# Kernel tuning notes

Hardware: AMD Instinct MI355X
Metric: run time of the kernel (lower is better)

## Reference

```python
import jax, jax.numpy as jnp
import numpy as np

DIM = 1024
HEADS = 16
HEAD_DIM = DIM // HEADS
SCALE = HEAD_DIM ** -0.5


def setup_inputs() -> dict:
    key = jax.random.key(0)
    ks = jax.random.split(key, 7)
    B, N, M = 2, 2048, 2048
    x = jax.random.normal(ks[0], (B, N, DIM), dtype=jnp.float32)
    y = jax.random.normal(ks[1], (B, M, DIM), dtype=jnp.float32)
    s = DIM ** -0.5
    Wq = jax.random.normal(ks[2], (DIM, DIM), dtype=jnp.float32) * s
    Wk = jax.random.normal(ks[3], (DIM, DIM), dtype=jnp.float32) * s
    Wv = jax.random.normal(ks[4], (DIM, DIM), dtype=jnp.float32) * s
    Wp = jax.random.normal(ks[5], (DIM, DIM), dtype=jnp.float32) * s
    bp = jax.random.normal(ks[6], (DIM,), dtype=jnp.float32) * 0.01
    return {"x": x, "y": y, "Wq": Wq, "Wk": Wk, "Wv": Wv, "Wp": Wp, "bp": bp}


def _split_heads(t):
    b, n, _ = t.shape
    return t.reshape(b, n, HEADS, HEAD_DIM).transpose(0, 2, 1, 3)  # b h n d


def reference(x, y, Wq, Wk, Wv, Wp, bp):
    q = _split_heads(x @ Wq)  # [b,h,n,d]
    k = _split_heads(y @ Wk)  # [b,h,m,d]
    v = _split_heads(y @ Wv)  # [b,h,m,d]
    attn = jnp.einsum('bhid,bhjd->bhij', q, k) * SCALE  # [b,h,n,m]
    attn = jax.nn.softmax(attn, axis=-1)
    out = jnp.einsum('bhij,bhjd->bhid', attn, v)  # [b,h,n,d]
    b, h, n, d = out.shape
    out = out.transpose(0, 2, 1, 3).reshape(b, n, h * d)  # [b,n,dim]
    return out @ Wp + bp
```

## Files before the change

kernel.cpp:

```cpp
#include <hip/hip_runtime.h>
#include <hip/hip_bf16.h>
#include <cstdint>

#define DIM   1024
#define HEADS 16
#define HDIM  64
#define BATCH 2
#define SEQ   2048
#define ROWS  (BATCH*SEQ)
static constexpr float QSCALE = 0.18033688f;

typedef float  f32x4  __attribute__((ext_vector_type(4)));
typedef float  float4v __attribute__((ext_vector_type(4)));
typedef __bf16 bf16x8 __attribute__((ext_vector_type(8)));
typedef __bf16 bf16x4 __attribute__((ext_vector_type(4)));
typedef short  short4v __attribute__((ext_vector_type(4)));

#if __has_builtin(__builtin_amdgcn_mfma_f32_16x16x16_bf16)
__device__ __forceinline__ f32x4 mfma16(bf16x4 a, bf16x4 b, f32x4 c) {
  return __builtin_amdgcn_mfma_f32_16x16x16_bf16(a, b, c, 0, 0, 0);
}
#else
__device__ __forceinline__ f32x4 mfma16(bf16x4 a, bf16x4 b, f32x4 c) {
  return __builtin_amdgcn_mfma_f32_16x16x16bf16_1k(
      __builtin_bit_cast(short4v, a), __builtin_bit_cast(short4v, b), c, 0, 0, 0);
}
#endif

__device__ __forceinline__ void glds16(const __bf16* g, __bf16* l) {
  __builtin_amdgcn_global_load_lds(
      (const __attribute__((address_space(1))) void*)g,
      (__attribute__((address_space(3))) void*)l, 16, 0, 0);
}

__global__ __launch_bounds__(256) void prep_kernel(
    const float* __restrict__ x, const float* __restrict__ y,
    const float* __restrict__ Wq, const float* __restrict__ Wk,
    const float* __restrict__ Wv, const float* __restrict__ Wp,
    __bf16* __restrict__ xb, __bf16* __restrict__ yb, __bf16* __restrict__ Wt) {
  const int z = blockIdx.z, t = threadIdx.x;
  const size_t NEL = (size_t)ROWS * DIM;
  if (z < 8) {
    size_t idx = (((size_t)z * 1024 + blockIdx.x) * 256 + t) * 4;
    const float* s; __bf16* d;
    if (idx < NEL) { s = x + idx; d = xb + idx; }
    else           { s = y + (idx - NEL); d = yb + (idx - NEL); }
    const float4v v = *(const float4v*)s;
    bf16x4 o;
    o[0] = (__bf16)v[0]; o[1] = (__bf16)v[1]; o[2] = (__bf16)v[2]; o[3] = (__bf16)v[3];
    *(bf16x4*)d = o;
    return;
  }
  const int w = blockIdx.x >> 8, rem = blockIdx.x & 255;
  const float* W = (w == 0) ? Wq : (w == 1) ? Wk : (w == 2) ? Wv : Wp;
  __bf16* dst = Wt + (size_t)w * DIM * DIM;
  const int n0 = (rem & 15) * 64, k0 = (rem >> 4) * 64;
  __shared__ float T[64][65];
  const int col = t & 63, rw = t >> 6;
  #pragma unroll
  for (int p = 0; p < 16; ++p) {
    const int row = p * 4 + rw;
    T[row][col] = W[(size_t)(k0 + row) * DIM + n0 + col];
  }
  __syncthreads();
  #pragma unroll
  for (int p = 0; p < 16; ++p) {
    const int row = p * 4 + rw;
    dst[(size_t)(n0 + row) * DIM + k0 + col] = (__bf16)T[col][row];
  }
}

__global__ __launch_bounds__(256) void proj_kernel(
    const __bf16* __restrict__ xb, const __bf16* __restrict__ yb,
    const __bf16* __restrict__ Wt,
    __bf16* __restrict__ Qb, __bf16* __restrict__ Kb, __bf16* __restrict__ VT) {
  const int z = blockIdx.z;
  const __bf16* A = (z == 0) ? xb : yb;
  const __bf16* Bt = Wt + (size_t)z * DIM * DIM;

  __shared__ __bf16 S[2][128 * 64];
  __bf16* As = S[0];
  __bf16* Bs = S[1];

  const int t = threadIdx.x, lane = t & 63, wave = t >> 6;
  const int l15 = lane & 15, quad = lane >> 4;
  const int wm = wave & 1, wn = wave >> 1;
  const int rowBase = blockIdx.y * 128, colBase = blockIdx.x * 128;
  const int srow = lane >> 3;
  const int scol = ((lane & 7) ^ srow) * 8;

  f32x4 acc[4][4] = {};

  for (int kb = 0; kb < DIM; kb += 64) {
    __syncthreads();
    #pragma unroll
    for (int i = 0; i < 4; ++i) {
      const int c = wave * 4 + i;
      const int row = c * 8 + srow;
      glds16(&A[(size_t)(rowBase + row) * DIM + kb + scol], &As[c * 512]);
      glds16(&Bt[(size_t)(colBase + row) * DIM + kb + scol], &Bs[c * 512]);
    }
    __syncthreads();
    #pragma unroll
    for (int ks = 0; ks < 2; ++ks) {
      bf16x8 a[4], b[4];
      #pragma unroll
      for (int mi = 0; mi < 4; ++mi) {
        const int row = wm * 64 + mi * 16 + l15;
        a[mi] = *(const bf16x8*)&As[row * 64 + (((ks << 2) | quad) ^ (row & 7)) * 8];
      }
      #pragma unroll
      for (int ni = 0; ni < 4; ++ni) {
        const int row = wn * 64 + ni * 16 + l15;
        b[ni] = *(const bf16x8*)&Bs[row * 64 + (((ks << 2) | quad) ^ (row & 7)) * 8];
      }
      #pragma unroll
      for (int mi = 0; mi < 4; ++mi)
        #pragma unroll
        for (int ni = 0; ni < 4; ++ni)
          acc[mi][ni] = __builtin_amdgcn_mfma_f32_16x16x32_bf16(a[mi], b[ni], acc[mi][ni], 0, 0, 0);
    }
  }

  if (z < 2) {
    __bf16* out = (z == 0) ? Qb : Kb;
    const float sc = (z == 0) ? QSCALE : 1.0f;
    #pragma unroll
    for (int mi = 0; mi < 4; ++mi) {
      const int row0 = rowBase + wm * 64 + mi * 16 + quad * 4;
      #pragma unroll
      for (int ni = 0; ni < 4; ++ni) {
        const int col = colBase + wn * 64 + ni * 16 + l15;
        #pragma unroll
        for (int r = 0; r < 4; ++r)
          out[(size_t)(row0 + r) * DIM + col] = (__bf16)(acc[mi][ni][r] * sc);
      }
    }
    return;
  }

  __syncthreads();
  __bf16* Ts = &S[0][0];
  #pragma unroll
  for (int mi = 0; mi < 4; ++mi) {
    const int bk3 = wm * 8 + mi * 2 + (quad >> 1);
    #pragma unroll
    for (int ni = 0; ni < 4; ++ni) {
      const int dl = wn * 64 + ni * 16 + l15;
      bf16x4 pk;
      #pragma unroll
      for (int r = 0; r < 4; ++r) pk[r] = (__bf16)acc[mi][ni][r];
      *(bf16x4*)&Ts[dl * 128 + (bk3 ^ (dl & 7)) * 8 + (quad & 1) * 4] = pk;
    }
  }
  __syncthreads();
  const int d = t >> 1, khh = t & 1;
  const size_t vrow = (size_t)((rowBase >> 11) * HEADS * HDIM) + colBase + d;
  const int key0g = rowBase & (SEQ - 1);
  #pragma unroll
  for (int j = 0; j < 8; ++j) {
    const int kc = khh * 8 + j;
    const int lc = (kc & 8) | ((kc ^ d) & 7);
    const bf16x8 v = *(const bf16x8*)&Ts[d * 128 + lc * 8];
    *(bf16x8*)&VT[vrow * SEQ + key0g + kc * 8] = v;
  }
}

__global__ __launch_bounds__(256, 2) void attn_kernel(
    const __bf16* __restrict__ Qb, const __bf16* __restrict__ Kb,
    const __bf16* __restrict__ VT, __bf16* __restrict__ Ob) {
  __shared__ __bf16 KV[2][2][64 * 64];
  __shared__ float lb[2][128];

  const int t = threadIdx.x, lane = t & 63, wave = t >> 6;
  const int l15 = lane & 15, quad = lane >> 4;
  const int bh = blockIdx.y, b = bh >> 4, h = bh & 15;
  const int qseg = wave & 1, kh = wave >> 1;
  const int qrow0 = blockIdx.x * 128 + qseg * 64;
  const int srow = lane >> 3;
  const int scol = ((lane & 7) ^ srow) * 8;

  const __bf16* Kbh = Kb + (size_t)b * SEQ * DIM + h * HDIM;
  const __bf16* Vbh = VT + (size_t)bh * HDIM * SEQ;

  bf16x8 qf[4][2];
  #pragma unroll
  for (int mi = 0; mi < 4; ++mi)
    #pragma unroll
    for (int ks = 0; ks < 2; ++ks)
      qf[mi][ks] = *(const bf16x8*)&Qb[(size_t)(b * SEQ + qrow0 + mi * 16 + l15) * DIM
                                       + h * HDIM + ks * 32 + quad * 8];

  bf16x4 ones4;
  #pragma unroll
  for (int i = 0; i < 4; ++i) ones4[i] = (__bf16)1.0f;

  f32x4 o[4][4] = {};
  f32x4 lacc[4] = {};

  auto stage = [&](int jb, int buf) {
    #pragma unroll
    for (int i = 0; i < 2; ++i) {
      const int c = wave * 2 + i;
      const int row = c * 8 + srow;
      glds16(&Kbh[(size_t)(jb + row) * DIM + scol], &KV[buf][0][c * 512]);
      glds16(&Vbh[(size_t)row * SEQ + jb + scol], &KV[buf][1][c * 512]);
    }
  };

  stage(0, 0);
  for (int j = 0; j < SEQ / 64; ++j) {
    const int buf = j & 1;
    __syncthreads();
    if (j + 1 < SEQ / 64) stage((j + 1) * 64, buf ^ 1);
    const __bf16* Ks = KV[buf][0];
    const __bf16* Vs = KV[buf][1];

    f32x4 sT[2][4] = {};
    #pragma unroll
    for (int ks = 0; ks < 2; ++ks)
      #pragma unroll
      for (int ni = 0; ni < 2; ++ni) {
        const int key = kh * 32 + ni * 16 + l15;
        const bf16x8 kf = *(const bf16x8*)&Ks[key * 64 + (((ks << 2) | quad) ^ (key & 7)) * 8];
        #pragma unroll
        for (int mi = 0; mi < 4; ++mi)
          sT[ni][mi] = __builtin_amdgcn_mfma_f32_16x16x32_bf16(kf, qf[mi][ks], sT[ni][mi], 0, 0, 0);
      }

    bf16x4 pa[2][4];
    #pragma unroll
    for (int ni = 0; ni < 2; ++ni)
      #pragma unroll
      for (int mi = 0; mi < 4; ++mi)
        #pragma unroll
        for (int r = 0; r < 4; ++r)
          pa[ni][mi][r] = (__bf16)__builtin_amdgcn_exp2f(sT[ni][mi][r]);

    #pragma unroll
    for (int ni = 0; ni < 2; ++ni) {
      const int key0 = kh * 32 + ni * 16;
      #pragma unroll
      for (int mi = 0; mi < 4; ++mi)
        lacc[mi] = mfma16(pa[ni][mi], ones4, lacc[mi]);
      #pragma unroll
      for (int dt = 0; dt < 4; ++dt) {
        const int d = dt * 16 + l15;
        const bf16x4 vf = *(const bf16x4*)&Vs[d * 64
            + (((key0 >> 3) + (quad >> 1)) ^ (d & 7)) * 8 + (quad & 1) * 4];
        #pragma unroll
        for (int mi = 0; mi < 4; ++mi)
          o[mi][dt] = mfma16(pa[ni][mi], vf, o[mi][dt]);
      }
    }
  }

  __syncthreads();
  float* mb = (float*)&KV[0][0][0];
  if (l15 == 0) {
    #pragma unroll
    for (int mi = 0; mi < 4; ++mi)
      #pragma unroll
      for (int r = 0; r < 4; ++r)
        lb[kh][qseg * 64 + mi * 16 + quad * 4 + r] = lacc[mi][r];
  }
  if (kh == 1) {
    #pragma unroll
    for (int mi = 0; mi < 4; ++mi)
      #pragma unroll
      for (int r = 0; r < 4; ++r) {
        const int q = mi * 16 + quad * 4 + r;
        #pragma unroll
        for (int dt = 0; dt < 4; ++dt)
          mb[qseg * 4096 + q * 64 + dt * 16 + l15] = o[mi][dt][r];
      }
  }
  __syncthreads();
  if (kh == 0) {
    #pragma unroll
    for (int mi = 0; mi < 4; ++mi)
      #pragma unroll
      for (int r = 0; r < 4; ++r) {
        const int q = mi * 16 + quad * 4 + r;
        const float inv = 1.f / (lb[0][qseg * 64 + q] + lb[1][qseg * 64 + q]);
        const size_t row = (size_t)(b * SEQ + qrow0 + q);
        #pragma unroll
        for (int dt = 0; dt < 4; ++dt) {
          const float ov = o[mi][dt][r] + mb[qseg * 4096 + q * 64 + dt * 16 + l15];
          Ob[row * DIM + h * HDIM + dt * 16 + l15] = (__bf16)(ov * inv);
        }
      }
  }
}

__global__ __launch_bounds__(256) void outproj_kernel(
    const __bf16* __restrict__ A, const __bf16* __restrict__ Bt,
    const float* __restrict__ bias, float* __restrict__ out) {
  __shared__ __bf16 As[64 * 64];
  __shared__ __bf16 Bs[128 * 64];

  const int t = threadIdx.x, lane = t & 63, wave = t >> 6;
  const int l15 = lane & 15, quad = lane >> 4;
  const int wm = wave & 1, wn = wave >> 1;
  const int rowBase = blockIdx.y * 64, colBase = blockIdx.x * 128;
  const int srow = lane >> 3;
  const int scol = ((lane & 7) ^ srow) * 8;

  f32x4 acc[2][4] = {};

  for (int kb = 0; kb < DIM; kb += 64) {
    __syncthreads();
    #pragma unroll
    for (int i = 0; i < 2; ++i) {
      const int c = wave * 2 + i;
      const int row = c * 8 + srow;
      glds16(&A[(size_t)(rowBase + row) * DIM + kb + scol], &As[c * 512]);
    }
    #pragma unroll
    for (int i = 0; i < 4; ++i) {
      const int c = wave * 4 + i;
      const int row = c * 8 + srow;
      glds16(&Bt[(size_t)(colBase + row) * DIM + kb + scol], &Bs[c * 512]);
    }
    __syncthreads();
    #pragma unroll
    for (int ks = 0; ks < 2; ++ks) {
      bf16x8 a[2], b[4];
      #pragma unroll
      for (int mi = 0; mi < 2; ++mi) {
        const int row = wm * 32 + mi * 16 + l15;
        a[mi] = *(const bf16x8*)&As[row * 64 + (((ks << 2) | quad) ^ (row & 7)) * 8];
      }
      #pragma unroll
      for (int ni = 0; ni < 4; ++ni) {
        const int row = wn * 64 + ni * 16 + l15;
        b[ni] = *(const bf16x8*)&Bs[row * 64 + (((ks << 2) | quad) ^ (row & 7)) * 8];
      }
      #pragma unroll
      for (int mi = 0; mi < 2; ++mi)
        #pragma unroll
        for (int ni = 0; ni < 4; ++ni)
          acc[mi][ni] = __builtin_amdgcn_mfma_f32_16x16x32_bf16(a[mi], b[ni], acc[mi][ni], 0, 0, 0);
    }
  }

  #pragma unroll
  for (int mi = 0; mi < 2; ++mi) {
    const int row0 = rowBase + wm * 32 + mi * 16 + quad * 4;
    #pragma unroll
    for (int ni = 0; ni < 4; ++ni) {
      const int col = colBase + wn * 64 + ni * 16 + l15;
      const float bb = bias[col];
      #pragma unroll
      for (int r = 0; r < 4; ++r)
        out[(size_t)(row0 + r) * DIM + col] = acc[mi][ni][r] + bb;
    }
  }
}

extern "C" void kernel_launch(void* const* d_in, const int* in_sizes, int n_in,
                              void* d_out, int out_size, void* d_ws, size_t ws_size,
                              hipStream_t stream) {
  const float* x  = (const float*)d_in[0];
  const float* y  = (const float*)d_in[1];
  const float* Wq = (const float*)d_in[2];
  const float* Wk = (const float*)d_in[3];
  const float* Wv = (const float*)d_in[4];
  const float* Wp = (const float*)d_in[5];
  const float* bp = (const float*)d_in[6];
  float* out = (float*)d_out;

  const size_t NEL = (size_t)ROWS * DIM;
  __bf16* xb = (__bf16*)d_ws;
  __bf16* yb = xb + NEL;
  __bf16* Wt = yb + NEL;
  __bf16* Qb = Wt + NEL;
  __bf16* Kb = Qb + NEL;
  __bf16* VT = Kb + NEL;
  __bf16* Ob = xb;

  prep_kernel<<<dim3(1024, 1, 9), 256, 0, stream>>>(x, y, Wq, Wk, Wv, Wp, xb, yb, Wt);
  proj_kernel<<<dim3(DIM / 128, ROWS / 128, 3), 256, 0, stream>>>(xb, yb, Wt, Qb, Kb, VT);
  attn_kernel<<<dim3(SEQ / 128, BATCH * HEADS), 256, 0, stream>>>(Qb, Kb, VT, Ob);
  outproj_kernel<<<dim3(DIM / 128, ROWS / 64), 256, 0, stream>>>(Ob, Wt + 3 * NEL / 4, bp, out);
}
```

Baseline: 212.4 us.

## Halve attention query tile, raise occupancy, compute row sums via shuffles

Shrinks the per-block query tile in the attention kernel from 128 to 64 rows. This doubles the grid to 1024 blocks, flattened to 1D with heads innermost, and launch bounds ask for 4 blocks per CU. The softmax denominator is now accumulated with scalar adds plus cross-lane shuffles instead of an extra MFMA against a ones vector. The aim is better latency hiding and CU fill, at the cost of each K/V tile being loaded and reused for half as many queries, which doubles K/V traffic.

```diff
diff --git a/kernel.cpp b/kernel.cpp
--- a/kernel.cpp
+++ b/kernel.cpp
@@ -166,37 +166,34 @@
   }
 }
 
-__global__ __launch_bounds__(256, 2) void attn_kernel(
+__global__ __launch_bounds__(256, 4) void attn_kernel(
     const __bf16* __restrict__ Qb, const __bf16* __restrict__ Kb,
     const __bf16* __restrict__ VT, __bf16* __restrict__ Ob) {
   __shared__ __bf16 KV[2][2][64 * 64];
-  __shared__ float lb[2][128];
+  __shared__ float lb[2][64];
 
   const int t = threadIdx.x, lane = t & 63, wave = t >> 6;
   const int l15 = lane & 15, quad = lane >> 4;
-  const int bh = blockIdx.y, b = bh >> 4, h = bh & 15;
+  const int bh = blockIdx.x & 31, qx = blockIdx.x >> 5;
+  const int b = bh >> 4, h = bh & 15;
   const int qseg = wave & 1, kh = wave >> 1;
-  const int qrow0 = blockIdx.x * 128 + qseg * 64;
+  const int qrow0 = qx * 64 + qseg * 32;
   const int srow = lane >> 3;
   const int scol = ((lane & 7) ^ srow) * 8;
 
   const __bf16* Kbh = Kb + (size_t)b * SEQ * DIM + h * HDIM;
   const __bf16* Vbh = VT + (size_t)bh * HDIM * SEQ;
 
-  bf16x8 qf[4][2];
-  #pragma unroll
-  for (int mi = 0; mi < 4; ++mi)
+  bf16x8 qf[2][2];
+  #pragma unroll
+  for (int mi = 0; mi < 2; ++mi)
     #pragma unroll
     for (int ks = 0; ks < 2; ++ks)
       qf[mi][ks] = *(const bf16x8*)&Qb[(size_t)(b * SEQ + qrow0 + mi * 16 + l15) * DIM
                                        + h * HDIM + ks * 32 + quad * 8];
 
-  bf16x4 ones4;
-  #pragma unroll
-  for (int i = 0; i < 4; ++i) ones4[i] = (__bf16)1.0f;
-
-  f32x4 o[4][4] = {};
-  f32x4 lacc[4] = {};
+  f32x4 o[2][4] = {};
+  float lsum[2] = {};
 
   auto stage = [&](int jb, int buf) {
     #pragma unroll
@@ -216,7 +213,7 @@
     const __bf16* Ks = KV[buf][0];
     const __bf16* Vs = KV[buf][1];
 
-    f32x4 sT[2][4] = {};
+    f32x4 sT[2][2] = {};
     #pragma unroll
     for (int ks = 0; ks < 2; ++ks)
       #pragma unroll
@@ -224,69 +221,72 @@
         const int key = kh * 32 + ni * 16 + l15;
         const bf16x8 kf = *(const bf16x8*)&Ks[key * 64 + (((ks << 2) | quad) ^ (key & 7)) * 8];
         #pragma unroll
-        for (int mi = 0; mi < 4; ++mi)
+        for (int mi = 0; mi < 2; ++mi)
           sT[ni][mi] = __builtin_amdgcn_mfma_f32_16x16x32_bf16(kf, qf[mi][ks], sT[ni][mi], 0, 0, 0);
       }
 
-    bf16x4 pa[2][4];
+    bf16x4 pa[2][2];
     #pragma unroll
     for (int ni = 0; ni < 2; ++ni)
       #pragma unroll
-      for (int mi = 0; mi < 4; ++mi)
-        #pragma unroll
-        for (int r = 0; r < 4; ++r)
-          pa[ni][mi][r] = (__bf16)__builtin_amdgcn_exp2f(sT[ni][mi][r]);
+      for (int mi = 0; mi < 2; ++mi)
+        #pragma unroll
+        for (int r = 0; r < 4; ++r) {
+          const float pv = __builtin_amdgcn_exp2f(sT[ni][mi][r]);
+          lsum[mi] += pv;
+          pa[ni][mi][r] = (__bf16)pv;
+        }
 
     #pragma unroll
     for (int ni = 0; ni < 2; ++ni) {
       const int key0 = kh * 32 + ni * 16;
-      #pragma unroll
-      for (int mi = 0; mi < 4; ++mi)
-        lacc[mi] = mfma16(pa[ni][mi], ones4, lacc[mi]);
       #pragma unroll
       for (int dt = 0; dt < 4; ++dt) {
         const int d = dt * 16 + l15;
         const bf16x4 vf = *(const bf16x4*)&Vs[d * 64
             + (((key0 >> 3) + (quad >> 1)) ^ (d & 7)) * 8 + (quad & 1) * 4];
         #pragma unroll
-        for (int mi = 0; mi < 4; ++mi)
+        for (int mi = 0; mi < 2; ++mi)
           o[mi][dt] = mfma16(pa[ni][mi], vf, o[mi][dt]);
       }
     }
   }
 
+  #pragma unroll
+  for (int mi = 0; mi < 2; ++mi) {
+    lsum[mi] += __shfl_xor(lsum[mi], 16, 64);
+    lsum[mi] += __shfl_xor(lsum[mi], 32, 64);
+  }
   __syncthreads();
   float* mb = (float*)&KV[0][0][0];
-  if (l15 == 0) {
-    #pragma unroll
-    for (int mi = 0; mi < 4; ++mi)
-      #pragma unroll
-      for (int r = 0; r < 4; ++r)
-        lb[kh][qseg * 64 + mi * 16 + quad * 4 + r] = lacc[mi][r];
+  if (quad == 0) {
+    #pragma unroll
+    for (int mi = 0; mi < 2; ++mi)
+      lb[kh][qseg * 32 + mi * 16 + l15] = lsum[mi];
   }
   if (kh == 1) {
     #pragma unroll
-    for (int mi = 0; mi < 4; ++mi)
+    for (int mi = 0; mi < 2; ++mi)
       #pragma unroll
       for (int r = 0; r < 4; ++r) {
-        const int q = mi * 16 + quad * 4 + r;
+        const int q = qseg * 32 + mi * 16 + quad * 4 + r;
         #pragma unroll
         for (int dt = 0; dt < 4; ++dt)
-          mb[qseg * 4096 + q * 64 + dt * 16 + l15] = o[mi][dt][r];
+          mb[q * 64 + dt * 16 + l15] = o[mi][dt][r];
       }
   }
   __syncthreads();
   if (kh == 0) {
     #pragma unroll
-    for (int mi = 0; mi < 4; ++mi)
+    for (int mi = 0; mi < 2; ++mi)
       #pragma unroll
       for (int r = 0; r < 4; ++r) {
-        const int q = mi * 16 + quad * 4 + r;
-        const float inv = 1.f / (lb[0][qseg * 64 + q] + lb[1][qseg * 64 + q]);
-        const size_t row = (size_t)(b * SEQ + qrow0 + q);
+        const int q = qseg * 32 + mi * 16 + quad * 4 + r;
+        const float inv = 1.f / (lb[0][q] + lb[1][q]);
+        const size_t row = (size_t)(b * SEQ + qx * 64 + q);
         #pragma unroll
         for (int dt = 0; dt < 4; ++dt) {
-          const float ov = o[mi][dt][r] + mb[qseg * 4096 + q * 64 + dt * 16 + l15];
+          const float ov = o[mi][dt][r] + mb[q * 64 + dt * 16 + l15];
           Ob[row * DIM + h * HDIM + dt * 16 + l15] = (__bf16)(ov * inv);
         }
       }
@@ -381,6 +381,6 @@
 
   prep_kernel<<<dim3(1024, 1, 9), 256, 0, stream>>>(x, y, Wq, Wk, Wv, Wp, xb, yb, Wt);
   proj_kernel<<<dim3(DIM / 128, ROWS / 128, 3), 256, 0, stream>>>(xb, yb, Wt, Qb, Kb, VT);
-  attn_kernel<<<dim3(SEQ / 128, BATCH * HEADS), 256, 0, stream>>>(Qb, Kb, VT, Ob);
+  attn_kernel<<<dim3((SEQ / 64) * BATCH * HEADS), 256, 0, stream>>>(Qb, Kb, VT, Ob);
   outproj_kernel<<<dim3(DIM / 128, ROWS / 64), 256, 0, stream>>>(Ob, Wt + 3 * NEL / 4, bp, out);
 }
```

Result: no change. 212.9 us (+0.3%).
